# Performance work log

Hardware: AMD Instinct MI355X
Metric: run time of the kernel (lower is better)

The kernel has to match this reference:

```python
import jax, jax.numpy as jnp
import numpy as np

B, N, H, IN, OUT, AXES = 128, 32, 128, 1, 10, 4


def setup_inputs() -> dict:
    key = jax.random.key(0)
    ks = jax.random.split(key, 6)
    s = 0.05
    return {
        "x": jax.random.normal(ks[0], (B, N, N), jnp.float32),
        "Wx": jax.random.normal(ks[1], (AXES, IN, 3 * H), jnp.float32) * s,
        "U1": jax.random.normal(ks[2], (AXES, H, 3 * H), jnp.float32) * s,
        "U2": jax.random.normal(ks[3], (AXES, H, 3 * H), jnp.float32) * s,
        "b": jnp.zeros((AXES, 3 * H), jnp.float32),
        "Wo": jax.random.normal(ks[4], (AXES * H, OUT), jnp.float32) * s,
        "bo": jnp.zeros((OUT,), jnp.float32),
    }


def _mdgru_cell(xj, h_top, h_left, Wx, U1, U2, b):
    # xj: (B, IN); h_top/h_left: (B, H). Two-predecessor GRU cell.
    gx = xj @ Wx + b          # (B, 3H)
    g1 = h_top @ U1           # (B, 3H)
    g2 = h_left @ U2          # (B, 3H)
    xr, xz, xn = jnp.split(gx, 3, axis=-1)
    r1, z1, n1 = jnp.split(g1, 3, axis=-1)
    r2, z2, n2 = jnp.split(g2, 3, axis=-1)
    r = jax.nn.sigmoid(xr + r1 + r2)
    z = jax.nn.sigmoid(xz + z1 + z2)
    n = jnp.tanh(xn + r * (n1 + n2))
    return (1.0 - z) * n + z * 0.5 * (h_top + h_left)


def _scan_dir(img, Wx, U1, U2, b):
    # img: (N_rows, N_cols, B), oriented so scan runs top-left -> bottom-right.
    n_cols, bsz = img.shape[1], img.shape[2]
    h0 = jnp.zeros((bsz, H), img.dtype)

    def row_step(last_row, x_row):  # last_row: (N_cols, B, H); x_row: (N_cols, B)
        def col_step(h_left, inp):
            xj, h_top = inp
            h = _mdgru_cell(xj[:, None], h_top, h_left, Wx, U1, U2, b)
            return h, h
        _, row = jax.lax.scan(col_step, h0, (x_row, last_row))
        return row, row[-1]

    _, finals = jax.lax.scan(row_step, jnp.zeros((n_cols, bsz, H), img.dtype), img)
    return finals[-1]  # (B, H): hidden at the terminal corner


def reference(x, Wx, U1, U2, b, Wo, bo):
    # x: (B, N, N). Four diagonal scan directions via flips.
    flips = [(False, False), (True, False), (False, True), (True, True)]
    hs = []
    for a, (fi, fj) in enumerate(flips):
        xd = x
        if fi:
            xd = jnp.flip(xd, axis=1)
        if fj:
            xd = jnp.flip(xd, axis=2)
        img = jnp.transpose(xd, (1, 2, 0))  # (N_rows, N_cols, B)
        hs.append(_scan_dir(img, Wx[a], U1[a], U2[a], b[a]))
    final_hidden = jnp.concatenate(hs, axis=1)  # (B, 4H)
    return jax.nn.log_softmax(final_hidden @ Wo + bo, axis=1)
```

## Files before the change

### kernel.cpp

```cpp
#include <hip/hip_runtime.h>
#include <type_traits>


#define B_ 128
#define N_ 32
#define H_ 128
#define TH 384
#define KK 256

#define PLSTR 2640
#define BUFSTR 10560
#define XD_STEP 256

typedef float f32x4 __attribute__((ext_vector_type(4)));
typedef float f32x2 __attribute__((ext_vector_type(2)));

__device__ inline unsigned cvt2fp8(float a, float b) {
    return (unsigned)__builtin_amdgcn_cvt_pk_fp8_f32(a, b, 0, false);
}

#define NL2E -1.44269504088896f

__global__ void conv_u(const float* __restrict__ U1, const float* __restrict__ U2,
                       char* __restrict__ ub8) {
    __shared__ float t[32][33];
    int bx = blockIdx.x;
    int amat = bx / 48, tile = bx % 48;
    int kt = tile / 12, ntl = tile % 12;
    int a = amat >> 1, mat = amat & 1;
    int kk0 = kt * 32, n0 = ntl * 32;
    int tx = threadIdx.x, ty = threadIdx.y;
    const float* U = mat ? U2 : U1;
#pragma unroll
    for (int r = 0; r < 4; r++)
        t[ty + r * 8][tx] = U[(a * H_ + kk0 + ty + r * 8) * TH + n0 + tx];
    __syncthreads();
#pragma unroll
    for (int r = 0; r < 4; r++) {
        int n = n0 + ty + r * 8;
        int kkl = kk0 + tx;
        unsigned pk = cvt2fp8(t[tx][ty + r * 8], 0.0f);
        ub8[(a * TH + n) * KK + mat * H_ + kkl] = (char)(pk & 0xFF);
    }
}

__global__ __launch_bounds__(512, 2) void scan_all(
    const float* __restrict__ x, const float* __restrict__ Wx,
    const float* __restrict__ bvec, const char* __restrict__ ubf8,
    float* __restrict__ finals) {

    __shared__ __align__(16) char hbf_c[2 * BUFSTR];
    __shared__ __align__(16) char xd_c[63 * XD_STEP];

    int bx = blockIdx.x;
    int a = bx >> 6, chunk = bx & 63;
    int tid = threadIdx.x;
    int lane = tid & 63, wn = tid >> 6;
    int l16 = lane & 15, lg = lane >> 4;

    for (int idx = tid; idx < (2 * BUFSTR) / 4; idx += 512) ((unsigned*)hbf_c)[idx] = 0u;
    for (int idx = tid; idx < (63 * XD_STEP) / 4; idx += 512) ((unsigned*)xd_c)[idx] = 0u;
    __syncthreads();

    const float* xg = x + (chunk * 2) * (N_ * N_);
    for (int cell = tid; cell < 1024; cell += 512) {
        int i = cell >> 5, j = cell & 31;
        int ri = (a & 1) ? (31 - i) : i;
        int cj = (a & 2) ? (31 - j) : j;
        float v0 = xg[ri * 32 + cj];
        float v1 = xg[1024 + ri * 32 + cj];
        *(float2*)(xd_c + (i + j) * XD_STEP + i * 8) = make_float2(v0, v1);
    }

    const char* ub = ubf8 + a * (TH * KK);
    long Bf[3][8];
#pragma unroll
    for (int p = 0; p < 3; p++) {
        int n = p * H_ + wn * 16 + l16;
#pragma unroll
        for (int ks = 0; ks < 8; ks++) {
            Bf[p][ks] = *(const long*)(ub + n * KK + ks * 32 + lg * 8);
            asm volatile("" : "+v"(Bf[p][ks]));
        }
    }

    int hh = wn * 16 + l16;
    float wxp[3], bsp[3];
    {
        float wr = Wx[a * TH + hh], br = bvec[a * TH + hh];
        float wz = Wx[a * TH + H_ + hh], bz = bvec[a * TH + H_ + hh];
        float wq = Wx[a * TH + 2 * H_ + hh], bq = bvec[a * TH + 2 * H_ + hh];
        wxp[0] = wr * NL2E; bsp[0] = br * NL2E;
        wxp[1] = wz * NL2E; bsp[1] = bz * NL2E;
        wxp[2] = wq;        bsp[2] = bq;
    }

    int aT[4], wbs[4];
#pragma unroll
    for (int mt = 0; mt < 4; mt++) {
        aT[mt] = (mt * 16 + l16) * 40 + lg * 8;
        wbs[mt] = (wn >> 1) * PLSTR + ((mt * 8 + lg * 2 + 1) * 2) * 40 +
                  (wn & 1) * 16 + l16;
    }

    const char* xdp = xd_c + lg * 16;
    __syncthreads();

    float hp[4][2][2];
#pragma unroll
    for (int mt = 0; mt < 4; mt++)
#pragma unroll
        for (int p2 = 0; p2 < 2; p2++)
#pragma unroll
            for (int bl = 0; bl < 2; bl++) hp[mt][p2][bl] = 0.0f;

    int slsrc = (lane - 16) & 63;

    auto step = [&](int d, auto WRC) {
        constexpr int WRB = decltype(WRC)::value;
        constexpr int RDB = WRB ^ 1;
        const char* hbr = hbf_c + RDB * BUFSTR;
        char* hbw = hbf_c + WRB * BUFSTR;

        bool gm[4];
        f32x4 xv[4];
#pragma unroll
        for (int mt = 0; mt < 4; mt++) {
            gm[mt] = (d >= mt * 8) && (d <= mt * 8 + 38);
            if (gm[mt]) xv[mt] = *(const f32x4*)(xdp + WRB * 256 + mt * 64);
        }

        float sh[4][2];
#pragma unroll
        for (int mt = 0; mt < 4; mt++) {
            bool need = gm[mt] || (mt < 3 && gm[mt + 1]);
            if (need) {
#pragma unroll
                for (int bl = 0; bl < 2; bl++)
                    sh[mt][bl] = __shfl(hp[mt][1][bl], slsrc, 64);
            }
        }

        f32x4 acc[4][3];
        const f32x4 z4 = {0.0f, 0.0f, 0.0f, 0.0f};

        auto do_mfma = [&](int mt) {
            long af[8];
#pragma unroll
            for (int ks = 0; ks < 4; ks++) {
                af[ks] = *(const long*)(hbr + ks * PLSTR + aT[mt]);
                af[ks + 4] = *(const long*)(hbr + ks * PLSTR + aT[mt] + 80);
            }
#pragma unroll
            for (int ks = 0; ks < 4; ks++)
#pragma unroll
                for (int p = 0; p < 3; p++)
                    acc[mt][p] = __builtin_amdgcn_mfma_f32_16x16x32_fp8_fp8(
                        af[ks], Bf[p][ks], (ks == 0) ? z4 : acc[mt][p], 0, 0, 0);
#pragma unroll
            for (int ks = 0; ks < 4; ks++)
#pragma unroll
                for (int p = 0; p < 3; p++)
                    acc[mt][p] = __builtin_amdgcn_mfma_f32_16x16x32_fp8_fp8(
                        af[ks + 4], Bf[p][ks + 4], acc[mt][p], 0, 0, 0);
        };

        auto do_epi = [&](int mt) {
            f32x2 top0;
            if (mt == 0)
                top0 = lg ? (f32x2){sh[0][0], sh[0][1]} : (f32x2){0.0f, 0.0f};
            else
                top0 = lg ? (f32x2){sh[mt][0], sh[mt][1]}
                          : (f32x2){sh[mt - 1][0], sh[mt - 1][1]};
#pragma unroll
            for (int p2 = 0; p2 < 2; p2++) {
                f32x2 xb = {xv[mt][p2 * 2], xv[mt][p2 * 2 + 1]};
                f32x2 Gr = {acc[mt][0][p2 * 2], acc[mt][0][p2 * 2 + 1]};
                f32x2 Gz = {acc[mt][1][p2 * 2], acc[mt][1][p2 * 2 + 1]};
                f32x2 Gn = {acc[mt][2][p2 * 2], acc[mt][2][p2 * 2 + 1]};
                f32x2 htop = p2 ? (f32x2){hp[mt][0][0], hp[mt][0][1]} : top0;
                f32x2 hlft = {hp[mt][p2][0], hp[mt][p2][1]};
                f32x2 ar = Gr * NL2E + (xb * wxp[0] + bsp[0]);
                f32x2 rg;
                rg.x = __builtin_amdgcn_rcpf(1.0f + __builtin_amdgcn_exp2f(ar.x));
                rg.y = __builtin_amdgcn_rcpf(1.0f + __builtin_amdgcn_exp2f(ar.y));
                f32x2 az = Gz * NL2E + (xb * wxp[1] + bsp[1]);
                f32x2 ezv;
                ezv.x = __builtin_amdgcn_exp2f(az.x);
                ezv.y = __builtin_amdgcn_exp2f(az.y);
                f32x2 vn = rg * Gn + (xb * wxp[2] + bsp[2]);
                f32x2 vn2 = vn * (2.0f * NL2E);
                f32x2 env;
                env.x = __builtin_amdgcn_exp2f(vn2.x);
                env.y = __builtin_amdgcn_exp2f(vn2.y);
                f32x2 pz = ezv + 1.0f, pn = env + 1.0f;
                f32x2 pzn = pz * pn;
                f32x2 rp;
                rp.x = __builtin_amdgcn_rcpf(pzn.x);
                rp.y = __builtin_amdgcn_rcpf(pzn.y);
                f32x2 zg = rp * pn;
                f32x2 ng = (rp * 2.0f) * pz - 1.0f;
                f32x2 hs = htop + hlft;
                f32x2 t = ng - hs * 0.5f;
                f32x2 hv = ng - zg * t;
                unsigned pk = cvt2fp8(hv.x, hv.y);
                char* wp = hbw + wbs[mt] + p2 * 80;
                wp[0] = (char)(pk & 0xFF);
                wp[40] = (char)((pk >> 8) & 0xFF);
                hp[mt][p2][0] = hv.x;
                hp[mt][p2][1] = hv.y;
            }
        };

        if (gm[0]) do_mfma(0);
        if (gm[1]) do_mfma(1);
        if (gm[0]) do_epi(0);
        if (gm[2]) do_mfma(2);
        if (gm[1]) do_epi(1);
        if (gm[3]) do_mfma(3);
        if (gm[2]) do_epi(2);
        if (gm[3]) do_epi(3);

        __syncthreads();
    };

    for (int d = 0; d < 62; d += 2) {
        step(d, std::integral_constant<int, 0>{});
        step(d + 1, std::integral_constant<int, 1>{});
        xdp += 512;
    }
    step(62, std::integral_constant<int, 0>{});

    if (lg == 3) {
        finals[(a * B_ + chunk * 2) * H_ + hh] = hp[3][1][0];
        finals[(a * B_ + chunk * 2 + 1) * H_ + hh] = hp[3][1][1];
    }
}

__global__ void classify(const float* __restrict__ fin, const float* __restrict__ Wo,
                         const float* __restrict__ bo, float* __restrict__ out) {
    int b = blockIdx.x;
    int lane = threadIdx.x;
    float acc[10];
#pragma unroll
    for (int o = 0; o < 10; o++) acc[o] = 0.0f;
#pragma unroll
    for (int kkx = 0; kkx < 8; kkx++) {
        int k = kkx * 64 + lane;
        int a = k >> 7, hh = k & 127;
        float fh = fin[(a * B_ + b) * H_ + hh];
#pragma unroll
        for (int o = 0; o < 10; o++) acc[o] += fh * Wo[k * 10 + o];
    }
    float logits[10];
#pragma unroll
    for (int o = 0; o < 10; o++) {
        float v = acc[o];
#pragma unroll
        for (int off = 32; off; off >>= 1) v += __shfl_xor(v, off, 64);
        logits[o] = v + bo[o];
    }
    float m = logits[0];
#pragma unroll
    for (int o = 1; o < 10; o++) m = fmaxf(m, logits[o]);
    float s = 0.0f;
#pragma unroll
    for (int o = 0; o < 10; o++) s += __expf(logits[o] - m);
    float lse = m + __logf(s);
    if (lane == 0) {
#pragma unroll
        for (int o = 0; o < 10; o++) out[b * 10 + o] = logits[o] - lse;
    }
}

extern "C" void kernel_launch(void* const* d_in, const int* in_sizes, int n_in,
                              void* d_out, int out_size, void* d_ws, size_t ws_size,
                              hipStream_t stream) {
    const float* x = (const float*)d_in[0];
    const float* Wx = (const float*)d_in[1];
    const float* U1 = (const float*)d_in[2];
    const float* U2 = (const float*)d_in[3];
    const float* bv = (const float*)d_in[4];
    const float* Wo = (const float*)d_in[5];
    const float* bo = (const float*)d_in[6];
    float* out = (float*)d_out;

    char* ws = (char*)d_ws;
    char* ub8 = ws;
    float* finals = (float*)(ws + 393216);

    hipLaunchKernelGGL(conv_u, dim3(384), dim3(32, 8), 0, stream, U1, U2, ub8);
    hipLaunchKernelGGL(scan_all, dim3(256), dim3(512), 0, stream, x, Wx, bv, ub8, finals);
    hipLaunchKernelGGL(classify, dim3(128), dim3(64), 0, stream, finals, Wo, bo, out);
}
```

Measured before the change: 145.6 us.

## Compute all four MFMA tiles unconditionally each wavefront step, masking only writes

Drops the per-tile active-diagonal branches around loads, shuffles, MFMAs and epilogue, so every step computes all four row tiles. The loop over k-steps is reordered to interleave tiles, giving the scheduler branch-free straight-line code with independent MFMA chains. Only the final state writeback stays conditional on the tile being active. This removes divergence and serialization overhead but adds redundant MFMA and transcendental work on steps near the start and end of the diagonal sweep, and it raises register pressure from holding all A fragments at once.

After: 173.2 us. +19.0%, slower.

```diff
diff --git a/kernel.cpp b/kernel.cpp
--- a/kernel.cpp
+++ b/kernel.cpp
@@ -127,45 +127,39 @@
 #pragma unroll
         for (int mt = 0; mt < 4; mt++) {
             gm[mt] = (d >= mt * 8) && (d <= mt * 8 + 38);
-            if (gm[mt]) xv[mt] = *(const f32x4*)(xdp + WRB * 256 + mt * 64);
+            xv[mt] = *(const f32x4*)(xdp + WRB * 256 + mt * 64);
         }
 
         float sh[4][2];
 #pragma unroll
-        for (int mt = 0; mt < 4; mt++) {
-            bool need = gm[mt] || (mt < 3 && gm[mt + 1]);
-            if (need) {
-#pragma unroll
-                for (int bl = 0; bl < 2; bl++)
-                    sh[mt][bl] = __shfl(hp[mt][1][bl], slsrc, 64);
+        for (int mt = 0; mt < 4; mt++)
+#pragma unroll
+            for (int bl = 0; bl < 2; bl++)
+                sh[mt][bl] = __shfl(hp[mt][1][bl], slsrc, 64);
+
+        long af[4][8];
+#pragma unroll
+        for (int mt = 0; mt < 4; mt++)
+#pragma unroll
+            for (int ks = 0; ks < 4; ks++) {
+                af[mt][ks] = *(const long*)(hbr + ks * PLSTR + aT[mt]);
+                af[mt][ks + 4] = *(const long*)(hbr + ks * PLSTR + aT[mt] + 80);
             }
-        }
 
         f32x4 acc[4][3];
         const f32x4 z4 = {0.0f, 0.0f, 0.0f, 0.0f};
-
-        auto do_mfma = [&](int mt) {
-            long af[8];
-#pragma unroll
-            for (int ks = 0; ks < 4; ks++) {
-                af[ks] = *(const long*)(hbr + ks * PLSTR + aT[mt]);
-                af[ks + 4] = *(const long*)(hbr + ks * PLSTR + aT[mt] + 80);
-            }
-#pragma unroll
-            for (int ks = 0; ks < 4; ks++)
+#pragma unroll
+        for (int ks = 0; ks < 8; ks++)
+#pragma unroll
+            for (int mt = 0; mt < 4; mt++)
 #pragma unroll
                 for (int p = 0; p < 3; p++)
                     acc[mt][p] = __builtin_amdgcn_mfma_f32_16x16x32_fp8_fp8(
-                        af[ks], Bf[p][ks], (ks == 0) ? z4 : acc[mt][p], 0, 0, 0);
-#pragma unroll
-            for (int ks = 0; ks < 4; ks++)
-#pragma unroll
-                for (int p = 0; p < 3; p++)
-                    acc[mt][p] = __builtin_amdgcn_mfma_f32_16x16x32_fp8_fp8(
-                        af[ks + 4], Bf[p][ks + 4], acc[mt][p], 0, 0, 0);
-        };
-
-        auto do_epi = [&](int mt) {
+                        af[mt][ks], Bf[p][ks], (ks == 0) ? z4 : acc[mt][p], 0, 0, 0);
+
+        f32x2 hv[4][2];
+#pragma unroll
+        for (int mt = 0; mt < 4; mt++) {
             f32x2 top0;
             if (mt == 0)
                 top0 = lg ? (f32x2){sh[0][0], sh[0][1]} : (f32x2){0.0f, 0.0f};
@@ -202,25 +196,23 @@
                 f32x2 ng = (rp * 2.0f) * pz - 1.0f;
                 f32x2 hs = htop + hlft;
                 f32x2 t = ng - hs * 0.5f;
-                f32x2 hv = ng - zg * t;
-                unsigned pk = cvt2fp8(hv.x, hv.y);
-                char* wp = hbw + wbs[mt] + p2 * 80;
-                wp[0] = (char)(pk & 0xFF);
-                wp[40] = (char)((pk >> 8) & 0xFF);
-                hp[mt][p2][0] = hv.x;
-                hp[mt][p2][1] = hv.y;
+                hv[mt][p2] = ng - zg * t;
             }
-        };
-
-        if (gm[0]) do_mfma(0);
-        if (gm[1]) do_mfma(1);
-        if (gm[0]) do_epi(0);
-        if (gm[2]) do_mfma(2);
-        if (gm[1]) do_epi(1);
-        if (gm[3]) do_mfma(3);
-        if (gm[2]) do_epi(2);
-        if (gm[3]) do_epi(3);
-
+        }
+#pragma unroll
+        for (int mt = 0; mt < 4; mt++) {
+            if (gm[mt]) {
+#pragma unroll
+                for (int p2 = 0; p2 < 2; p2++) {
+                    unsigned pk = cvt2fp8(hv[mt][p2].x, hv[mt][p2].y);
+                    char* wp = hbw + wbs[mt] + p2 * 80;
+                    wp[0] = (char)(pk & 0xFF);
+                    wp[40] = (char)((pk >> 8) & 0xFF);
+                    hp[mt][p2][0] = hv[mt][p2].x;
+                    hp[mt][p2][1] = hv[mt][p2].y;
+                }
+            }
+        }
         __syncthreads();
     };
 
```
